# Kernel tuning notes

Measured on AMD Instinct MI355X. Metric: run time of the kernel, lower is better.

Reference implementation:

```python
import jax, jax.numpy as jnp
import numpy as np

S, B, E, H = 1024, 4, 1024, 16
D = E // H  # head_dim = 64


def setup_inputs() -> dict:
    key = jax.random.key(0)
    ks = jax.random.split(key, 22)
    inp = {}
    names_io = ["query_r", "query_i", "key_r", "key_i", "value_r", "value_i"]
    for i, n in enumerate(names_io):
        inp[n] = jax.random.normal(ks[i], (S, B, E), dtype=jnp.float32)
    scale = 0.02
    j = 6
    for p in ["q", "k", "v", "o"]:
        inp[f"w{p}_r"] = jax.random.normal(ks[j], (E, E), dtype=jnp.float32) * scale; j += 1
        inp[f"w{p}_i"] = jax.random.normal(ks[j], (E, E), dtype=jnp.float32) * scale; j += 1
        inp[f"b{p}_r"] = jax.random.normal(ks[j], (E,), dtype=jnp.float32) * scale; j += 1
        inp[f"b{p}_i"] = jax.random.normal(ks[j], (E,), dtype=jnp.float32) * scale; j += 1
    return inp


def _clinear(x, wr, wi, br, bi):
    # complex linear: x @ W^T + b, torch Linear convention (weight [out,in])
    w = wr + 1j * wi
    b = br + 1j * bi
    return x @ w.T + b


def reference(query_r, query_i, key_r, key_i, value_r, value_i,
              wq_r, wq_i, bq_r, bq_i, wk_r, wk_i, bk_r, bk_i,
              wv_r, wv_i, bv_r, bv_i, wo_r, wo_i, bo_r, bo_i):
    # batch_first=False: inputs are [S, B, E] -> [B, S, E]
    q = jnp.transpose(query_r + 1j * query_i, (1, 0, 2))
    k = jnp.transpose(key_r + 1j * key_i, (1, 0, 2))
    v = jnp.transpose(value_r + 1j * value_i, (1, 0, 2))

    def heads(x):  # [B,S,E] -> [B,H,S,D]
        return jnp.transpose(x.reshape(B, S, H, D), (0, 2, 1, 3))

    Q = heads(_clinear(q, wq_r, wq_i, bq_r, bq_i))
    K = heads(_clinear(k, wk_r, wk_i, bk_r, bk_i))
    V = heads(_clinear(v, wv_r, wv_i, bv_r, bv_i))

    scores = jnp.einsum("bhqd,bhkd->bhqk", Q, K) / jnp.sqrt(jnp.float32(D))
    # split softmax: softmax over real and imag parts independently
    attn = (jax.nn.softmax(scores.real, axis=-1)
            + 1j * jax.nn.softmax(scores.imag, axis=-1))
    out = jnp.einsum("bhqk,bhkd->bhqd", attn, V)  # [B,H,S,D]
    out = jnp.transpose(out, (0, 2, 1, 3)).reshape(B, S, E)
    out = _clinear(out, wo_r, wo_i, bo_r, bo_i)
    out = jnp.transpose(out, (1, 0, 2))  # back to [S,B,E]
    # return complex output as stacked (real, imag) floats: [S,B,E,2]
    return jnp.stack([out.real, out.imag], axis=-1)
```

## Files before the change

### kernel.cpp

```cpp
#include <hip/hip_runtime.h>
#include <hip/hip_bf16.h>
#include <stdint.h>

#define S_LEN 1024
#define B_SZ  4
#define E_SZ  1024
#define H_CNT 16
#define D_HD  64
#define N1    (B_SZ * H_CNT * S_LEN * D_HD)
#define WELEM (E_SZ * E_SZ)

typedef __attribute__((ext_vector_type(8))) short short8;
typedef __attribute__((ext_vector_type(4))) float f32x4;

__device__ __forceinline__ ushort f2bf(float f) {
  union { float f; uint32_t u; } v; v.f = f;
  uint32_t u = v.u;
  uint32_t r = (u + 0x7fffu + ((u >> 16) & 1u)) >> 16;
  return (ushort)r;
}
__device__ __forceinline__ float bf2f(ushort u) {
  union { uint32_t u; float f; } v; v.u = ((uint32_t)u) << 16;
  return v.f;
}
__device__ __forceinline__ short8 pack8(float4 a, float4 b) {
  short8 r;
  r[0] = (short)f2bf(a.x); r[1] = (short)f2bf(a.y);
  r[2] = (short)f2bf(a.z); r[3] = (short)f2bf(a.w);
  r[4] = (short)f2bf(b.x); r[5] = (short)f2bf(b.y);
  r[6] = (short)f2bf(b.z); r[7] = (short)f2bf(b.w);
  return r;
}
static __device__ __forceinline__ f32x4 mfma16(short8 a, short8 b, f32x4 c) {
  return __builtin_amdgcn_mfma_f32_16x16x32_bf16(a, b, c, 0, 0, 0);
}

typedef const __attribute__((address_space(1))) void gv_t;
typedef __attribute__((address_space(3))) void lv_t;
__device__ __forceinline__ void gld16(const void* g, void* l) {
  __builtin_amdgcn_global_load_lds((gv_t*)g, (lv_t*)l, 16, 0, 0);
}

__global__ __launch_bounds__(256) void cast_w8(
    const float* __restrict__ s0, const float* __restrict__ s1,
    const float* __restrict__ s2, const float* __restrict__ s3,
    const float* __restrict__ s4, const float* __restrict__ s5,
    const float* __restrict__ s6, const float* __restrict__ s7,
    ushort* __restrict__ dst)
{
  const size_t i = (size_t)blockIdx.x * blockDim.x + threadIdx.x;
  const size_t e = i * 4;
  const int which = (int)(e >> 20);
  const size_t off = e & (WELEM - 1);
  const float* s = which < 4
      ? (which < 2 ? (which == 0 ? s0 : s1) : (which == 2 ? s2 : s3))
      : (which < 6 ? (which == 4 ? s4 : s5) : (which == 6 ? s6 : s7));
  const float4 f = *(const float4*)(s + off);
  ushort4 u;
  u.x = f2bf(f.x); u.y = f2bf(f.y); u.z = f2bf(f.z); u.w = f2bf(f.w);
  *(ushort4*)(dst + e) = u;
}

__global__ __launch_bounds__(256) void castA2(
    const float* __restrict__ xr0, const float* __restrict__ xi0,
    const float* __restrict__ xr1, const float* __restrict__ xi1,
    ushort* __restrict__ yr0, ushort* __restrict__ yi0,
    ushort* __restrict__ yr1, ushort* __restrict__ yi1)
{
  int blk = blockIdx.x;
  const float *xr, *xi; ushort *yr, *yi;
  if (blk < 2048) { xr = xr0; xi = xi0; yr = yr0; yi = yi0; }
  else            { xr = xr1; xi = xi1; yr = yr1; yi = yi1; blk -= 2048; }
  const size_t e = ((size_t)blk * 256 + threadIdx.x) * 8;
  float4 a = *(const float4*)(xr + e);
  float4 b = *(const float4*)(xr + e + 4);
  *(short8*)(yr + e) = pack8(a, b);
  a = *(const float4*)(xi + e);
  b = *(const float4*)(xi + e + 4);
  *(short8*)(yi + e) = pack8(a, b);
}

__global__ __launch_bounds__(256) void castA(
    const float* __restrict__ xr, const float* __restrict__ xi,
    ushort* __restrict__ yr, ushort* __restrict__ yi)
{
  const size_t e = ((size_t)blockIdx.x * 256 + threadIdx.x) * 8;
  float4 a = *(const float4*)(xr + e);
  float4 b = *(const float4*)(xr + e + 4);
  *(short8*)(yr + e) = pack8(a, b);
  a = *(const float4*)(xi + e);
  b = *(const float4*)(xi + e + 4);
  *(short8*)(yi + e) = pack8(a, b);
}

template<int MODE>
__global__ __launch_bounds__(256) void cgemm(
    const ushort* __restrict__ ar_, const ushort* __restrict__ ai_,
    const ushort* __restrict__ wre, const ushort* __restrict__ wim,
    const float* __restrict__ bre, const float* __restrict__ bim,
    ushort* __restrict__ yr, ushort* __restrict__ yi,
    float* __restrict__ outf, float scale)
{
  __shared__ __align__(16) ushort sAr[128 * 64], sAi[128 * 64];
  __shared__ __align__(16) ushort sBr[64 * 64],  sBi[64 * 64];

  const int tid  = threadIdx.x;
  const int lane = tid & 63;
  const int w    = tid >> 6;
  const int wrow = w >> 1, wcol = w & 1;
  const int fr   = lane & 15, fq = lane >> 4;

  const int flat = blockIdx.x + gridDim.x * blockIdx.y;
  const int swz  = (flat & 7) * 64 + (flat >> 3);
  const int n0   = (swz & 15) * 64;
  const int m0   = (swz >> 4) * 128;

  const ushort* gbase = (w == 0) ? ar_ : (w == 1) ? ai_ : (w == 2) ? wre : wim;
  char* sbase = (w == 0) ? (char*)sAr : (w == 1) ? (char*)sAi
              : (w == 2) ? (char*)sBr : (char*)sBi;
  const int rbase = (w < 2) ? m0 : n0;
  const int lrow  = lane >> 3;
  const int sch   = (lane & 7) ^ lrow;
  const ushort* gp0 = gbase + (size_t)(rbase + lrow) * E_SZ + sch * 8;

  f32x4 accR[4][2] = {}, accI[4][2] = {};

  for (int kt = 0; kt < 16; ++kt) {
    const int k0 = kt * 64;
    __syncthreads();
    if (w < 2) {
#pragma unroll
      for (int i = 0; i < 16; ++i)
        gld16(gp0 + (size_t)i * 8 * E_SZ + k0, sbase + i * 1024);
    } else {
#pragma unroll
      for (int i = 0; i < 8; ++i)
        gld16(gp0 + (size_t)i * 8 * E_SZ + k0, sbase + i * 1024);
    }
    __syncthreads();

#pragma unroll
    for (int kk = 0; kk < 2; ++kk) {
      short8 a_r[4], a_i[4], a_n[4], b_r[2], b_i[2];
#pragma unroll
      for (int mi = 0; mi < 4; ++mi) {
        const int row = wrow * 64 + mi * 16 + fr;
        const int off = row * 128 + (((kk * 4 + fq) ^ (row & 7)) << 4);
        a_r[mi] = *(const short8*)((const char*)sAr + off);
        a_i[mi] = *(const short8*)((const char*)sAi + off);
        a_n[mi] = a_i[mi] ^ (short)0x8000;
      }
#pragma unroll
      for (int ni = 0; ni < 2; ++ni) {
        const int row = wcol * 32 + ni * 16 + fr;
        const int off = row * 128 + (((kk * 4 + fq) ^ (row & 7)) << 4);
        b_r[ni] = *(const short8*)((const char*)sBr + off);
        b_i[ni] = *(const short8*)((const char*)sBi + off);
      }
      __builtin_amdgcn_s_setprio(1);
#pragma unroll
      for (int mi = 0; mi < 4; ++mi)
#pragma unroll
        for (int ni = 0; ni < 2; ++ni) {
          accR[mi][ni] = mfma16(a_r[mi], b_r[ni], accR[mi][ni]);
          accR[mi][ni] = mfma16(a_n[mi], b_i[ni], accR[mi][ni]);
          accI[mi][ni] = mfma16(a_r[mi], b_i[ni], accI[mi][ni]);
          accI[mi][ni] = mfma16(a_i[mi], b_r[ni], accI[mi][ni]);
        }
      __builtin_amdgcn_s_setprio(0);
    }
  }

#pragma unroll
  for (int ni = 0; ni < 2; ++ni) {
    const int n = n0 + wcol * 32 + ni * 16 + fr;
    const float bR = bre[n], bI = bim[n];
    const int h = n >> 6, d = n & 63;
#pragma unroll
    for (int mi = 0; mi < 4; ++mi) {
      const int mb = m0 + wrow * 64 + mi * 16 + fq * 4;
#pragma unroll
      for (int q = 0; q < 4; ++q) {
        const int m = mb + q;
        const float vr = (accR[mi][ni][q] + bR) * scale;
        const float vi = (accI[mi][ni][q] + bI) * scale;
        if (MODE == 0) {
          const int s = m >> 2, b = m & 3;
          const size_t o = (((size_t)(b * H_CNT + h) * S_LEN) + s) * D_HD + d;
          yr[o] = f2bf(vr); yi[o] = f2bf(vi);
        } else if (MODE == 1) {
          const int s = m >> 2, b = m & 3;
          const size_t o = (((size_t)(b * H_CNT + h) * D_HD) + d) * S_LEN + s;
          yr[o] = f2bf(vr); yi[o] = f2bf(vi);
        } else {
          const int b = m >> 10, s = m & 1023;
          const size_t o = (((size_t)(s * B_SZ + b) * E_SZ) + n) * 2;
          outf[o] = vr; outf[o + 1] = vi;
        }
      }
    }
  }
}

__global__ __launch_bounds__(256) void cattn_mfma(
    const ushort* __restrict__ Qr, const ushort* __restrict__ Qi,
    const ushort* __restrict__ Kr, const ushort* __restrict__ Ki,
    const ushort* __restrict__ Vtr, const ushort* __restrict__ Vti,
    ushort* __restrict__ AOr, ushort* __restrict__ AOi)
{
  __shared__ __align__(16) ushort sK[2][64][64];
  __shared__ __align__(16) ushort sVt[2][64][64];
  __shared__ __align__(16) ushort sP[4][2][32][64];

  const int tid  = threadIdx.x;
  const int lane = tid & 63;
  const int w    = tid >> 6;
  const int g    = lane >> 4;
  const int fr   = lane & 15;
  const int bh   = blockIdx.y;
  const int b    = bh >> 4, h = bh & 15;
  const int q0   = blockIdx.x * 128;
  const int qw   = q0 + 32 * w;

  short8 qfr[2][2], qfi[2][2];
#pragma unroll
  for (int hq = 0; hq < 2; ++hq) {
    const size_t qrow = ((size_t)bh * S_LEN + qw + hq * 16 + fr) * D_HD;
#pragma unroll
    for (int kk = 0; kk < 2; ++kk) {
      qfr[hq][kk] = *(const short8*)(Qr + qrow + kk * 32 + g * 8);
      qfi[hq][kk] = *(const short8*)(Qi + qrow + kk * 32 + g * 8);
    }
  }

  const int lrow8 = lane >> 3;
  const int sch   = (lane & 7) ^ lrow8;
  const ushort* gsrc; ushort* sdst;
  if      (w == 0) { gsrc = Kr  + (size_t)bh * S_LEN * D_HD; sdst = &sK[0][0][0]; }
  else if (w == 1) { gsrc = Ki  + (size_t)bh * S_LEN * D_HD; sdst = &sK[1][0][0]; }
  else if (w == 2) { gsrc = Vtr + (size_t)bh * D_HD * S_LEN; sdst = &sVt[0][0][0]; }
  else             { gsrc = Vti + (size_t)bh * D_HD * S_LEN; sdst = &sVt[1][0][0]; }
  const bool isK = (w < 2);

  f32x4 accA[2][4] = {}, accAi[2][4] = {}, accB[2][4] = {}, accBi[2][4] = {};
  f32x4 lpr[2] = {}, lpi[2] = {};

  ushort* pR = &sP[w][0][0][0];
  ushort* pI = &sP[w][1][0][0];
  const int par  = fr & 1;
  const int k0b  = fr & ~1;
  ushort* pbuf   = par ? pI : pR;
  const int woff = (k0b * 2) & 15;

  if (isK) {
    const ushort* gp = gsrc + lrow8 * 64 + sch * 8;
#pragma unroll
    for (int i = 0; i < 8; ++i)
      gld16(gp + i * 512, (char*)sdst + i * 1024);
  }
  __syncthreads();

  for (int kt = 0; kt < 16; ++kt) {
    if (!isK) {
      const ushort* gp = gsrc + (size_t)lrow8 * S_LEN + kt * 64 + sch * 8;
#pragma unroll
      for (int i = 0; i < 8; ++i)
        gld16(gp + (size_t)i * 8 * S_LEN, (char*)sdst + i * 1024);
    }

    f32x4 Sr[2][4] = {}, Si[2][4] = {};
    __builtin_amdgcn_s_setprio(1);
#pragma unroll
    for (int n = 0; n < 4; ++n) {
      const int kc = fr + 16 * n;
      const int rb = kc * 128, sw = (kc & 7) << 4;
#pragma unroll
      for (int kk = 0; kk < 2; ++kk) {
        const int off = rb + ((((kk * 4 + g) << 4)) ^ sw);
        short8 krf = *(const short8*)((const char*)&sK[0][0][0] + off);
        short8 kif = *(const short8*)((const char*)&sK[1][0][0] + off);
        short8 kin = kif ^ (short)0x8000;
#pragma unroll
        for (int hq = 0; hq < 2; ++hq) {
          Sr[hq][n] = mfma16(qfr[hq][kk], krf, Sr[hq][n]);
          Sr[hq][n] = mfma16(qfi[hq][kk], kin, Sr[hq][n]);
          Si[hq][n] = mfma16(qfr[hq][kk], kif, Si[hq][n]);
          Si[hq][n] = mfma16(qfi[hq][kk], krf, Si[hq][n]);
        }
      }
    }
    __builtin_amdgcn_s_setprio(0);

#pragma unroll
    for (int hq = 0; hq < 2; ++hq)
#pragma unroll
      for (int n = 0; n < 4; ++n) {
        const int cbase = (k0b + 16 * n) >> 3;
#pragma unroll
        for (int t = 0; t < 4; ++t) {
          float pr = __expf(Sr[hq][n][t]);
          float pi = __expf(Si[hq][n][t]);
          lpr[hq][t] += pr; lpi[hq][t] += pi;
          float pro = __shfl_xor(pr, 1);
          float pio = __shfl_xor(pi, 1);
          float lo = par ? pio : pr;
          float hi = par ? pi  : pro;
          uint32_t pk;
          asm("v_cvt_pk_bf16_f32 %0, %1, %2" : "=v"(pk) : "v"(lo), "v"(hi));
          const int q = hq * 16 + g * 4 + t;
          const int off = q * 128 + ((cbase ^ (q & 7)) << 4) + woff;
          *(uint32_t*)((char*)pbuf + off) = pk;
        }
      }

    __syncthreads();

    if (isK && kt < 15) {
      const ushort* gp = gsrc + (size_t)(kt + 1) * 4096 + lrow8 * 64 + sch * 8;
#pragma unroll
      for (int i = 0; i < 8; ++i)
        gld16(gp + i * 512, (char*)sdst + i * 1024);
    }

    short8 prf[2][2], pif[2][2];
#pragma unroll
    for (int hq = 0; hq < 2; ++hq)
#pragma unroll
      for (int kk = 0; kk < 2; ++kk) {
        const int off = (hq * 16 + fr) * 128 + ((((kk * 4 + g) << 4)) ^ ((fr & 7) << 4));
        prf[hq][kk] = *(const short8*)((const char*)pR + off);
        pif[hq][kk] = *(const short8*)((const char*)pI + off);
      }
    __builtin_amdgcn_s_setprio(1);
#pragma unroll
    for (int n = 0; n < 4; ++n) {
      const int d = fr + 16 * n;
      const int rb = d * 128, sw = (d & 7) << 4;
#pragma unroll
      for (int kk = 0; kk < 2; ++kk) {
        const int off = rb + ((((kk * 4 + g) << 4)) ^ sw);
        short8 vrf = *(const short8*)((const char*)&sVt[0][0][0] + off);
        short8 vif = *(const short8*)((const char*)&sVt[1][0][0] + off);
#pragma unroll
        for (int hq = 0; hq < 2; ++hq) {
          accA [hq][n] = mfma16(prf[hq][kk], vrf, accA [hq][n]);
          accAi[hq][n] = mfma16(prf[hq][kk], vif, accAi[hq][n]);
          accB [hq][n] = mfma16(pif[hq][kk], vrf, accB [hq][n]);
          accBi[hq][n] = mfma16(pif[hq][kk], vif, accBi[hq][n]);
        }
      }
    }
    __builtin_amdgcn_s_setprio(0);

    __syncthreads();
  }

#pragma unroll
  for (int mm = 1; mm < 16; mm <<= 1)
#pragma unroll
    for (int hq = 0; hq < 2; ++hq)
#pragma unroll
      for (int t = 0; t < 4; ++t) {
        lpr[hq][t] += __shfl_xor(lpr[hq][t], mm);
        lpi[hq][t] += __shfl_xor(lpi[hq][t], mm);
      }

#pragma unroll
  for (int hq = 0; hq < 2; ++hq) {
    f32x4 ilr, ili;
#pragma unroll
    for (int t = 0; t < 4; ++t) { ilr[t] = 1.f / lpr[hq][t]; ili[t] = 1.f / lpi[hq][t]; }
#pragma unroll
    for (int n = 0; n < 4; ++n) {
      const int e = h * 64 + fr + 16 * n;
#pragma unroll
      for (int t = 0; t < 4; ++t) {
        const int sidx = qw + hq * 16 + g * 4 + t;
        const size_t o = ((size_t)b * S_LEN + sidx) * E_SZ + e;
        AOr[o] = f2bf(accA [hq][n][t] * ilr[t] - accBi[hq][n][t] * ili[t]);
        AOi[o] = f2bf(accAi[hq][n][t] * ilr[t] + accB [hq][n][t] * ili[t]);
      }
    }
  }
}

extern "C" void kernel_launch(void* const* d_in, const int* in_sizes, int n_in,
                              void* d_out, int out_size, void* d_ws, size_t ws_size,
                              hipStream_t stream)
{
    const float* query_r = (const float*)d_in[0];
    const float* query_i = (const float*)d_in[1];
    const float* key_r   = (const float*)d_in[2];
    const float* key_i   = (const float*)d_in[3];
    const float* value_r = (const float*)d_in[4];
    const float* value_i = (const float*)d_in[5];
    const float* wq_r = (const float*)d_in[6];
    const float* wq_i = (const float*)d_in[7];
    const float* bq_r = (const float*)d_in[8];
    const float* bq_i = (const float*)d_in[9];
    const float* wk_r = (const float*)d_in[10];
    const float* wk_i = (const float*)d_in[11];
    const float* bk_r = (const float*)d_in[12];
    const float* bk_i = (const float*)d_in[13];
    const float* wv_r = (const float*)d_in[14];
    const float* wv_i = (const float*)d_in[15];
    const float* bv_r = (const float*)d_in[16];
    const float* bv_i = (const float*)d_in[17];
    const float* wo_r = (const float*)d_in[18];
    const float* wo_i = (const float*)d_in[19];
    const float* bo_r = (const float*)d_in[20];
    const float* bo_i = (const float*)d_in[21];

    ushort* ws   = (ushort*)d_ws;
    ushort* Qr   = ws;
    ushort* Qi   = Qr + (size_t)N1;
    ushort* Kr   = Qi + (size_t)N1;
    ushort* Ki   = Kr + (size_t)N1;
    ushort* Vtr  = Ki + (size_t)N1;
    ushort* Vti  = Vtr + (size_t)N1;
    ushort* Wb   = Vti + (size_t)N1;
    ushort* Wq_r = Wb + 0 * (size_t)WELEM;
    ushort* Wq_i = Wb + 1 * (size_t)WELEM;
    ushort* Wk_r = Wb + 2 * (size_t)WELEM;
    ushort* Wk_i = Wb + 3 * (size_t)WELEM;
    ushort* Wv_r = Wb + 4 * (size_t)WELEM;
    ushort* Wv_i = Wb + 5 * (size_t)WELEM;
    ushort* Wo_r = Wb + 6 * (size_t)WELEM;
    ushort* Wo_i = Wb + 7 * (size_t)WELEM;
    ushort* AOr  = Wb + 8 * (size_t)WELEM;
    ushort* AOi  = AOr + (size_t)N1;

    ushort* Xq_r = (ushort*)d_out;
    ushort* Xq_i = Xq_r + (size_t)N1;
    ushort* Xk_r = Xq_i + (size_t)N1;
    ushort* Xk_i = Xk_r + (size_t)N1;

    cast_w8<<<8192, 256, 0, stream>>>(wq_r, wq_i, wk_r, wk_i,
                                      wv_r, wv_i, wo_r, wo_i, Wb);
    castA2<<<4096, 256, 0, stream>>>(query_r, query_i, key_r, key_i,
                                     Xq_r, Xq_i, Xk_r, Xk_i);

    dim3 gg(16, 32);

    cgemm<0><<<gg, 256, 0, stream>>>(Xq_r, Xq_i, Wq_r, Wq_i, bq_r, bq_i,
                                     Qr, Qi, nullptr, 0.125f);
    cgemm<0><<<gg, 256, 0, stream>>>(Xk_r, Xk_i, Wk_r, Wk_i, bk_r, bk_i,
                                     Kr, Ki, nullptr, 1.0f);
    castA<<<2048, 256, 0, stream>>>(value_r, value_i, Xq_r, Xq_i);
    cgemm<1><<<gg, 256, 0, stream>>>(Xq_r, Xq_i, Wv_r, Wv_i, bv_r, bv_i,
                                     Vtr, Vti, nullptr, 1.0f);

    cattn_mfma<<<dim3(S_LEN / 128, B_SZ * H_CNT), 256, 0, stream>>>(
        Qr, Qi, Kr, Ki, Vtr, Vti, AOr, AOi);

    cgemm<2><<<gg, 256, 0, stream>>>(AOr, AOi, Wo_r, Wo_i, bo_r, bo_i,
                                     nullptr, nullptr, (float*)d_out, 1.0f);
}
```

Before: 318.7 us.

## Halve attention query tile per block, drop K prefetch, fold log2e into Q scale

The attention kernel now processes 64 query rows per block (16 per wave) instead of 128, doubling the grid and halving per-wave accumulator registers. Launch bounds request three blocks per SIMD so more waves stay resident. The K double-buffered prefetch is removed in favor of a load-then-sync at the start of every key tile, setprio hints are dropped, and the per-wave P scratch shrinks. The Q projection scale absorbs log2(e) so the softmax uses the native exp2. More blocks reload K/V tiles, doubling global K/V traffic, and there is less overlap of loads with compute.

```diff
diff --git a/kernel.cpp b/kernel.cpp
--- a/kernel.cpp
+++ b/kernel.cpp
@@ -18,10 +18,6 @@
   uint32_t u = v.u;
   uint32_t r = (u + 0x7fffu + ((u >> 16) & 1u)) >> 16;
   return (ushort)r;
-}
-__device__ __forceinline__ float bf2f(ushort u) {
-  union { uint32_t u; float f; } v; v.u = ((uint32_t)u) << 16;
-  return v.f;
 }
 __device__ __forceinline__ short8 pack8(float4 a, float4 b) {
   short8 r;
@@ -202,7 +198,7 @@
   }
 }
 
-__global__ __launch_bounds__(256) void cattn_mfma(
+__global__ __launch_bounds__(256, 3) void cattn_mfma(
     const ushort* __restrict__ Qr, const ushort* __restrict__ Qi,
     const ushort* __restrict__ Kr, const ushort* __restrict__ Ki,
     const ushort* __restrict__ Vtr, const ushort* __restrict__ Vti,
@@ -210,7 +206,7 @@
 {
   __shared__ __align__(16) ushort sK[2][64][64];
   __shared__ __align__(16) ushort sVt[2][64][64];
-  __shared__ __align__(16) ushort sP[4][2][32][64];
+  __shared__ __align__(16) ushort sP[4][2][16][64];
 
   const int tid  = threadIdx.x;
   const int lane = tid & 63;
@@ -219,18 +215,15 @@
   const int fr   = lane & 15;
   const int bh   = blockIdx.y;
   const int b    = bh >> 4, h = bh & 15;
-  const int q0   = blockIdx.x * 128;
-  const int qw   = q0 + 32 * w;
-
-  short8 qfr[2][2], qfi[2][2];
-#pragma unroll
-  for (int hq = 0; hq < 2; ++hq) {
-    const size_t qrow = ((size_t)bh * S_LEN + qw + hq * 16 + fr) * D_HD;
-#pragma unroll
-    for (int kk = 0; kk < 2; ++kk) {
-      qfr[hq][kk] = *(const short8*)(Qr + qrow + kk * 32 + g * 8);
-      qfi[hq][kk] = *(const short8*)(Qi + qrow + kk * 32 + g * 8);
-    }
+  const int q0   = blockIdx.x * 64;
+  const int qw   = q0 + 16 * w;
+
+  short8 qfr[2], qfi[2];
+  const size_t qrow = ((size_t)bh * S_LEN + qw + fr) * D_HD;
+#pragma unroll
+  for (int kk = 0; kk < 2; ++kk) {
+    qfr[kk] = *(const short8*)(Qr + qrow + kk * 32 + g * 8);
+    qfi[kk] = *(const short8*)(Qi + qrow + kk * 32 + g * 8);
   }
 
   const int lrow8 = lane >> 3;
@@ -242,8 +235,8 @@
   else             { gsrc = Vti + (size_t)bh * D_HD * S_LEN; sdst = &sVt[1][0][0]; }
   const bool isK = (w < 2);
 
-  f32x4 accA[2][4] = {}, accAi[2][4] = {}, accB[2][4] = {}, accBi[2][4] = {};
-  f32x4 lpr[2] = {}, lpi[2] = {};
+  f32x4 accA[4] = {}, accAi[4] = {}, accB[4] = {}, accBi[4] = {};
+  f32x4 lpr = {}, lpi = {};
 
   ushort* pR = &sP[w][0][0][0];
   ushort* pI = &sP[w][1][0][0];
@@ -252,24 +245,22 @@
   ushort* pbuf   = par ? pI : pR;
   const int woff = (k0b * 2) & 15;
 
-  if (isK) {
-    const ushort* gp = gsrc + lrow8 * 64 + sch * 8;
-#pragma unroll
-    for (int i = 0; i < 8; ++i)
-      gld16(gp + i * 512, (char*)sdst + i * 1024);
-  }
-  __syncthreads();
-
   for (int kt = 0; kt < 16; ++kt) {
-    if (!isK) {
+    __syncthreads();
+    if (isK) {
+      const ushort* gp = gsrc + (size_t)kt * 4096 + lrow8 * 64 + sch * 8;
+#pragma unroll
+      for (int i = 0; i < 8; ++i)
+        gld16(gp + i * 512, (char*)sdst + i * 1024);
+    } else {
       const ushort* gp = gsrc + (size_t)lrow8 * S_LEN + kt * 64 + sch * 8;
 #pragma unroll
       for (int i = 0; i < 8; ++i)
         gld16(gp + (size_t)i * 8 * S_LEN, (char*)sdst + i * 1024);
     }
-
-    f32x4 Sr[2][4] = {}, Si[2][4] = {};
-    __builtin_amdgcn_s_setprio(1);
+    __syncthreads();
+
+    f32x4 Sr[4] = {}, Si[4] = {};
 #pragma unroll
     for (int n = 0; n < 4; ++n) {
       const int kc = fr + 16 * n;
@@ -280,58 +271,41 @@
         short8 krf = *(const short8*)((const char*)&sK[0][0][0] + off);
         short8 kif = *(const short8*)((const char*)&sK[1][0][0] + off);
         short8 kin = kif ^ (short)0x8000;
-#pragma unroll
-        for (int hq = 0; hq < 2; ++hq) {
-          Sr[hq][n] = mfma16(qfr[hq][kk], krf, Sr[hq][n]);
-          Sr[hq][n] = mfma16(qfi[hq][kk], kin, Sr[hq][n]);
-          Si[hq][n] = mfma16(qfr[hq][kk], kif, Si[hq][n]);
-          Si[hq][n] = mfma16(qfi[hq][kk], krf, Si[hq][n]);
-        }
-      }
-    }
-    __builtin_amdgcn_s_setprio(0);
-
-#pragma unroll
-    for (int hq = 0; hq < 2; ++hq)
-#pragma unroll
-      for (int n = 0; n < 4; ++n) {
-        const int cbase = (k0b + 16 * n) >> 3;
-#pragma unroll
-        for (int t = 0; t < 4; ++t) {
-          float pr = __expf(Sr[hq][n][t]);
-          float pi = __expf(Si[hq][n][t]);
-          lpr[hq][t] += pr; lpi[hq][t] += pi;
-          float pro = __shfl_xor(pr, 1);
-          float pio = __shfl_xor(pi, 1);
-          float lo = par ? pio : pr;
-          float hi = par ? pi  : pro;
-          uint32_t pk;
-          asm("v_cvt_pk_bf16_f32 %0, %1, %2" : "=v"(pk) : "v"(lo), "v"(hi));
-          const int q = hq * 16 + g * 4 + t;
-          const int off = q * 128 + ((cbase ^ (q & 7)) << 4) + woff;
-          *(uint32_t*)((char*)pbuf + off) = pk;
-        }
-      }
-
-    __syncthreads();
-
-    if (isK && kt < 15) {
-      const ushort* gp = gsrc + (size_t)(kt + 1) * 4096 + lrow8 * 64 + sch * 8;
-#pragma unroll
-      for (int i = 0; i < 8; ++i)
-        gld16(gp + i * 512, (char*)sdst + i * 1024);
-    }
-
-    short8 prf[2][2], pif[2][2];
-#pragma unroll
-    for (int hq = 0; hq < 2; ++hq)
-#pragma unroll
-      for (int kk = 0; kk < 2; ++kk) {
-        const int off = (hq * 16 + fr) * 128 + ((((kk * 4 + g) << 4)) ^ ((fr & 7) << 4));
-        prf[hq][kk] = *(const short8*)((const char*)pR + off);
-        pif[hq][kk] = *(const short8*)((const char*)pI + off);
-      }
-    __builtin_amdgcn_s_setprio(1);
+        Sr[n] = mfma16(qfr[kk], krf, Sr[n]);
+        Sr[n] = mfma16(qfi[kk], kin, Sr[n]);
+        Si[n] = mfma16(qfr[kk], kif, Si[n]);
+        Si[n] = mfma16(qfi[kk], krf, Si[n]);
+      }
+    }
+
+#pragma unroll
+    for (int n = 0; n < 4; ++n) {
+      const int cbase = (k0b + 16 * n) >> 3;
+#pragma unroll
+      for (int t = 0; t < 4; ++t) {
+        float pr = __builtin_amdgcn_exp2f(Sr[n][t]);
+        float pi = __builtin_amdgcn_exp2f(Si[n][t]);
+        lpr[t] += pr; lpi[t] += pi;
+        float pro = __shfl_xor(pr, 1);
+        float pio = __shfl_xor(pi, 1);
+        float lo = par ? pio : pr;
+        float hi = par ? pi  : pro;
+        uint32_t pk;
+        asm("v_cvt_pk_bf16_f32 %0, %1, %2" : "=v"(pk) : "v"(lo), "v"(hi));
+        const int q = g * 4 + t;
+        const int off = q * 128 + ((cbase ^ (q & 7)) << 4) + woff;
+        *(uint32_t*)((char*)pbuf + off) = pk;
+      }
+    }
+    asm volatile("s_waitcnt lgkmcnt(0)" ::: "memory");
+
+    short8 prf[2], pif[2];
+#pragma unroll
+    for (int kk = 0; kk < 2; ++kk) {
+      const int off = fr * 128 + ((((kk * 4 + g) << 4)) ^ ((fr & 7) << 4));
+      prf[kk] = *(const short8*)((const char*)pR + off);
+      pif[kk] = *(const short8*)((const char*)pI + off);
+    }
 #pragma unroll
     for (int n = 0; n < 4; ++n) {
       const int d = fr + 16 * n;
@@ -341,45 +315,34 @@
         const int off = rb + ((((kk * 4 + g) << 4)) ^ sw);
         short8 vrf = *(const short8*)((const char*)&sVt[0][0][0] + off);
         short8 vif = *(const short8*)((const char*)&sVt[1][0][0] + off);
-#pragma unroll
-        for (int hq = 0; hq < 2; ++hq) {
-          accA [hq][n] = mfma16(prf[hq][kk], vrf, accA [hq][n]);
-          accAi[hq][n] = mfma16(prf[hq][kk], vif, accAi[hq][n]);
-          accB [hq][n] = mfma16(pif[hq][kk], vrf, accB [hq][n]);
-          accBi[hq][n] = mfma16(pif[hq][kk], vif, accBi[hq][n]);
-        }
-      }
-    }
-    __builtin_amdgcn_s_setprio(0);
-
-    __syncthreads();
+        accA [n] = mfma16(prf[kk], vrf, accA [n]);
+        accAi[n] = mfma16(prf[kk], vif, accAi[n]);
+        accB [n] = mfma16(pif[kk], vrf, accB [n]);
+        accBi[n] = mfma16(pif[kk], vif, accBi[n]);
+      }
+    }
   }
 
 #pragma unroll
   for (int mm = 1; mm < 16; mm <<= 1)
 #pragma unroll
-    for (int hq = 0; hq < 2; ++hq)
-#pragma unroll
-      for (int t = 0; t < 4; ++t) {
-        lpr[hq][t] += __shfl_xor(lpr[hq][t], mm);
-        lpi[hq][t] += __shfl_xor(lpi[hq][t], mm);
-      }
-
-#pragma unroll
-  for (int hq = 0; hq < 2; ++hq) {
-    f32x4 ilr, ili;
-#pragma unroll
-    for (int t = 0; t < 4; ++t) { ilr[t] = 1.f / lpr[hq][t]; ili[t] = 1.f / lpi[hq][t]; }
-#pragma unroll
-    for (int n = 0; n < 4; ++n) {
-      const int e = h * 64 + fr + 16 * n;
-#pragma unroll
-      for (int t = 0; t < 4; ++t) {
-        const int sidx = qw + hq * 16 + g * 4 + t;
-        const size_t o = ((size_t)b * S_LEN + sidx) * E_SZ + e;
-        AOr[o] = f2bf(accA [hq][n][t] * ilr[t] - accBi[hq][n][t] * ili[t]);
-        AOi[o] = f2bf(accAi[hq][n][t] * ilr[t] + accB [hq][n][t] * ili[t]);
-      }
+    for (int t = 0; t < 4; ++t) {
+      lpr[t] += __shfl_xor(lpr[t], mm);
+      lpi[t] += __shfl_xor(lpi[t], mm);
+    }
+
+  f32x4 ilr, ili;
+#pragma unroll
+  for (int t = 0; t < 4; ++t) { ilr[t] = 1.f / lpr[t]; ili[t] = 1.f / lpi[t]; }
+#pragma unroll
+  for (int n = 0; n < 4; ++n) {
+    const int e = h * 64 + fr + 16 * n;
+#pragma unroll
+    for (int t = 0; t < 4; ++t) {
+      const int sidx = qw + g * 4 + t;
+      const size_t o = ((size_t)b * S_LEN + sidx) * E_SZ + e;
+      AOr[o] = f2bf(accA [n][t] * ilr[t] - accBi[n][t] * ili[t]);
+      AOi[o] = f2bf(accAi[n][t] * ilr[t] + accB [n][t] * ili[t]);
     }
   }
 }
@@ -443,14 +406,14 @@
     dim3 gg(16, 32);
 
     cgemm<0><<<gg, 256, 0, stream>>>(Xq_r, Xq_i, Wq_r, Wq_i, bq_r, bq_i,
-                                     Qr, Qi, nullptr, 0.125f);
+                                     Qr, Qi, nullptr, 0.18033688011112043f);
     cgemm<0><<<gg, 256, 0, stream>>>(Xk_r, Xk_i, Wk_r, Wk_i, bk_r, bk_i,
                                      Kr, Ki, nullptr, 1.0f);
     castA<<<2048, 256, 0, stream>>>(value_r, value_i, Xq_r, Xq_i);
     cgemm<1><<<gg, 256, 0, stream>>>(Xq_r, Xq_i, Wv_r, Wv_i, bv_r, bv_i,
                                      Vtr, Vti, nullptr, 1.0f);
 
-    cattn_mfma<<<dim3(S_LEN / 128, B_SZ * H_CNT), 256, 0, stream>>>(
+    cattn_mfma<<<dim3(S_LEN / 64, B_SZ * H_CNT), 256, 0, stream>>>(
         Qr, Qi, Kr, Ki, Vtr, Vti, AOr, AOi);
 
     cgemm<2><<<gg, 256, 0, stream>>>(AOr, AOi, Wo_r, Wo_i, bo_r, bo_i,
```

Result: faster. 299.9 us (-5.9%).
